# Optimization experiments

Hardware: AMD Instinct MI355X
Metric: run time of the kernel (lower is better)

## Reference

```python
import jax, jax.numpy as jnp
import numpy as np

B, N, DIM = 2, 2048, 1024
H, DH = 16, 64            # num query heads, head dim (single shared kv head)
CTX_N, CTX_DIM = 256, 1024

def setup_inputs() -> dict:
    key = jax.random.key(0)
    ks = jax.random.split(key, 8)
    s = lambda fan: 1.0 / np.sqrt(fan)
    return {
        'x': jax.random.normal(ks[0], (B, N, DIM), jnp.float32),
        'context': jax.random.normal(ks[1], (B, CTX_N, CTX_DIM), jnp.float32),
        'g1': jnp.ones((DIM,), jnp.float32),
        'Wq': jax.random.normal(ks[2], (DIM, H * DH), jnp.float32) * s(DIM),
        'Wkv': jax.random.normal(ks[3], (DIM, 2 * DH), jnp.float32) * s(DIM),
        'null_kv': jax.random.normal(ks[4], (2, DH), jnp.float32) * s(DH),
        'ctx_g': jnp.ones((CTX_DIM,), jnp.float32),
        'ctx_b': jnp.zeros((CTX_DIM,), jnp.float32),
        'Wc': jax.random.normal(ks[5], (CTX_DIM, 2 * DH), jnp.float32) * s(CTX_DIM),
        'bc': jnp.zeros((2 * DH,), jnp.float32),
        'Wout': jax.random.normal(ks[6], (H * DH, DIM), jnp.float32) * s(H * DH),
        'g2': jnp.ones((DIM,), jnp.float32),
    }

def _ln_g(t, g, eps):
    # custom LayerNorm: scale only, no bias, population variance
    m = jnp.mean(t, axis=-1, keepdims=True)
    v = jnp.var(t, axis=-1, keepdims=True)
    return (t - m) / jnp.sqrt(v + eps) * g

def reference(x, context, g1, Wq, Wkv, null_kv, ctx_g, ctx_b, Wc, bc, Wout, g2):
    b, n, _ = x.shape
    scale = DH ** -0.5
    h = _ln_g(x, g1, 1e-5)                              # [b,n,dim]
    q = (h @ Wq).reshape(b, n, H, DH).transpose(0, 2, 1, 3) * scale  # [b,H,n,d]
    k, v = jnp.split(h @ Wkv, 2, axis=-1)               # each [b,n,d] (single kv head)
    # null kv token
    nk = jnp.broadcast_to(null_kv[0], (b, 1, DH))
    nv = jnp.broadcast_to(null_kv[1], (b, 1, DH))
    k = jnp.concatenate((k, nk), axis=-2)
    v = jnp.concatenate((v, nv), axis=-2)
    # context kv tokens (standard flax LayerNorm: scale+bias, eps=1e-6)
    cm = jnp.mean(context, axis=-1, keepdims=True)
    cv_ = jnp.var(context, axis=-1, keepdims=True)
    ch = (context - cm) / jnp.sqrt(cv_ + 1e-6) * ctx_g + ctx_b
    ck, cvv = jnp.split(ch @ Wc + bc, 2, axis=-1)       # [b,ctx_n,d]
    k = jnp.concatenate((k, ck), axis=-2)               # [b,j,d]
    v = jnp.concatenate((v, cvv), axis=-2)
    sim = jnp.einsum('bhid,bjd->bhij', q, k)            # shared kv head broadcast
    attn = jax.nn.softmax(sim, axis=-1)
    out = jnp.einsum('bhij,bjd->bhid', attn, v)
    out = out.transpose(0, 2, 1, 3).reshape(b, n, H * DH)
    out = out @ Wout
    return _ln_g(out, g2, 1e-5)
```

## Files before the change

### kernel.cpp

```cpp
#include <hip/hip_runtime.h>

typedef __attribute__((ext_vector_type(4)))  float  f32x4;
typedef __attribute__((ext_vector_type(16))) float  f32x16;
typedef __attribute__((ext_vector_type(8)))  short  s16x8;

#define DEVI __device__ __forceinline__

constexpr int Bb   = 2;
constexpr int Nn   = 2048;
constexpr int Hh   = 16;
constexpr int DHc  = 64;
constexpr int CTXN = 256;
constexpr int Jv   = Nn + 1 + CTXN;
constexpr int JP   = 2432;
constexpr int QKVN = Hh*DHc + 2*DHc;

DEVI unsigned short f2bf(float f) {
    union { float f; unsigned u; } v; v.f = f;
    unsigned r = v.u + 0x7fffu + ((v.u >> 16) & 1u);
    return (unsigned short)(r >> 16);
}
DEVI float bf2f(unsigned short h) {
    union { unsigned u; float f; } v; v.u = ((unsigned)h) << 16;
    return v.f;
}
DEVI unsigned cvt_pk_bf(float lo, float hi) {
    unsigned r;
    asm("v_cvt_pk_bf16_f32 %0, %1, %2" : "=v"(r) : "v"(lo), "v"(hi));
    return r;
}
DEVI float exp2v(float x) {
    float r;
    asm("v_exp_f32 %0, %1" : "=v"(r) : "v"(x));
    return r;
}
DEVI void gl_lds16(const void* g, void* l) {
    __builtin_amdgcn_global_load_lds(
        (__attribute__((address_space(1))) void*)g,
        (__attribute__((address_space(3))) void*)l,
        16, 0, 0);
}

__global__ __launch_bounds__(256) void k_pre(const float* __restrict__ Wq,
                                             const float* __restrict__ Wkv,
                                             const float* __restrict__ Wc,
                                             const float* __restrict__ Wout,
                                             const float* __restrict__ x,
                                             const float* __restrict__ ctx,
                                             const float* __restrict__ g1,
                                             const float* __restrict__ cg,
                                             const float* __restrict__ cb,
                                             unsigned short* __restrict__ WqkvT,
                                             unsigned short* __restrict__ WcT,
                                             unsigned short* __restrict__ WoutT,
                                             unsigned short* __restrict__ h,
                                             unsigned short* __restrict__ ch,
                                             float qscale) {
    int bxg = blockIdx.x;
    if (bxg < 2304) {
        __shared__ float tile[32][33];
        int bx = bxg % 72, by = bxg / 72;
        const float* in; unsigned short* out; int C; float scale; int cb_;
        if (bx < 32)      { in = Wq;   out = WqkvT;               C = 1024; scale = qscale; cb_ = bx; }
        else if (bx < 36) { in = Wkv;  out = WqkvT + 1024 * 1024; C = 128;  scale = 1.0f;  cb_ = bx - 32; }
        else if (bx < 40) { in = Wc;   out = WcT;                 C = 128;  scale = 1.0f;  cb_ = bx - 36; }
        else              { in = Wout; out = WoutT;               C = 1024; scale = 1.0f;  cb_ = bx - 40; }
        int tx = threadIdx.x & 31, ty = threadIdx.x >> 5;
        int r0 = by * 32, c0 = cb_ * 32;
#pragma unroll
        for (int i = 0; i < 32; i += 8)
            tile[ty + i][tx] = in[(size_t)(r0 + ty + i) * C + c0 + tx];
        __syncthreads();
#pragma unroll
        for (int i = 0; i < 32; i += 8)
            out[(size_t)(c0 + ty + i) * 1024 + r0 + tx] = f2bf(tile[tx][ty + i] * scale);
    } else {
        int row = bxg - 2304, tid = threadIdx.x;
        bool isx = row < 4096;
        const float* rp = isx ? x + (size_t)row * 1024 : ctx + (size_t)(row - 4096) * 1024;
        const float* g  = isx ? g1 : cg;
        float eps = isx ? 1e-5f : 1e-6f;
        unsigned short* o = isx ? h + (size_t)row * 1024 : ch + (size_t)(row - 4096) * 1024;

        f32x4 v = *(const f32x4*)(rp + tid * 4);
        float s = v.x + v.y + v.z + v.w;
        float q = v.x * v.x + v.y * v.y + v.z * v.z + v.w * v.w;
#pragma unroll
        for (int m = 32; m; m >>= 1) { s += __shfl_down(s, m, 64); q += __shfl_down(q, m, 64); }
        __shared__ float ss[4], sq[4];
        int wid = tid >> 6, lane = tid & 63;
        if (lane == 0) { ss[wid] = s; sq[wid] = q; }
        __syncthreads();
        s = ss[0] + ss[1] + ss[2] + ss[3];
        q = sq[0] + sq[1] + sq[2] + sq[3];
        float mean = s * (1.0f / 1024.0f);
        float var  = q * (1.0f / 1024.0f) - mean * mean;
        float rstd = rsqrtf(var + eps);
        f32x4 gg = *(const f32x4*)(g + tid * 4);
        f32x4 r;
#pragma unroll
        for (int e = 0; e < 4; e++) r[e] = (v[e] - mean) * rstd * gg[e];
        if (!isx) {
            f32x4 bb = *(const f32x4*)(cb + tid * 4);
#pragma unroll
            for (int e = 0; e < 4; e++) r[e] += bb[e];
        }
        uint2 ov = make_uint2(cvt_pk_bf(r[0], r[1]), cvt_pk_bf(r[2], r[3]));
        *(uint2*)(o + tid * 4) = ov;
    }
}

__global__ __launch_bounds__(256) void k_ln_out(const unsigned short* __restrict__ in,
                                                const float* __restrict__ g,
                                                float* __restrict__ out) {
    int row = blockIdx.x, tid = threadIdx.x;
    const unsigned short* rp = in + (size_t)row * 1024;
    uint2 raw = *(const uint2*)(rp + tid * 4);
    f32x4 v;
    v.x = bf2f((unsigned short)(raw.x & 0xffff));
    v.y = bf2f((unsigned short)(raw.x >> 16));
    v.z = bf2f((unsigned short)(raw.y & 0xffff));
    v.w = bf2f((unsigned short)(raw.y >> 16));
    float s = v.x + v.y + v.z + v.w;
    float q = v.x * v.x + v.y * v.y + v.z * v.z + v.w * v.w;
#pragma unroll
    for (int m = 32; m; m >>= 1) { s += __shfl_down(s, m, 64); q += __shfl_down(q, m, 64); }
    __shared__ float ss[4], sq[4];
    int wid = tid >> 6, lane = tid & 63;
    if (lane == 0) { ss[wid] = s; sq[wid] = q; }
    __syncthreads();
    s = ss[0] + ss[1] + ss[2] + ss[3];
    q = sq[0] + sq[1] + sq[2] + sq[3];
    float mean = s * (1.0f / 1024.0f);
    float var  = q * (1.0f / 1024.0f) - mean * mean;
    float rstd = rsqrtf(var + 1e-5f);
    f32x4 gg = *(const f32x4*)(g + tid * 4);
    f32x4 r;
#pragma unroll
    for (int e = 0; e < 4; e++) r[e] = (v[e] - mean) * rstd * gg[e];
    *(f32x4*)(out + (size_t)row * 1024 + tid * 4) = r;
}

template<int OUT_BF16>
DEVI void gemm_core(unsigned short* SAb, unsigned short* SBb,
                    const unsigned short* __restrict__ A,
                    const unsigned short* __restrict__ BT,
                    void* __restrict__ C,
                    int M, int N, int K, int bn, int bm) {
    int tid = threadIdx.x;
    int wid = tid >> 6, lane = tid & 63;
    int wm = wid >> 1, wn = wid & 1;
    int lr = lane & 15, lg = lane >> 4;
    int r8 = lane >> 3;
    int sl = (lane & 7) ^ r8;

    const unsigned short* Ag = A  + (size_t)(bm * 128 + wid * 32 + r8) * K + sl * 8;
    const unsigned short* Bg = BT + (size_t)(bn * 64  + wid * 16 + r8) * K + sl * 8;

    auto stage = [&](int buf, int s) {
        int k0 = s << 6;
        unsigned short* SA = SAb + buf * (128 * 64);
        unsigned short* SB = SBb + buf * (64 * 64);
#pragma unroll
        for (int i = 0; i < 4; i++)
            gl_lds16(Ag + (size_t)i * 8 * K + k0, SA + wid * 2048 + i * 512);
#pragma unroll
        for (int i = 0; i < 2; i++)
            gl_lds16(Bg + (size_t)i * 8 * K + k0, SB + wid * 1024 + i * 512);
    };

    f32x4 acc[4][2] = {};
    int nk = K >> 6;
    stage(0, 0);
    stage(1, 1);
    int b0 = 0;
#pragma unroll 1
    for (int s = 0; s < nk; ++s) {
        int b2 = b0 + 2; if (b2 >= 3) b2 -= 3;
        if (s + 2 < nk) {
            stage(b2, s + 2);
            asm volatile("s_waitcnt vmcnt(12)" ::: "memory");
        } else if (s + 1 < nk) {
            asm volatile("s_waitcnt vmcnt(6)" ::: "memory");
        } else {
            asm volatile("s_waitcnt vmcnt(0)" ::: "memory");
        }
        __builtin_amdgcn_s_barrier();
        __builtin_amdgcn_sched_barrier(0);
        const unsigned short* Al = SAb + b0 * (128 * 64);
        const unsigned short* Bl = SBb + b0 * (64 * 64);
#pragma unroll
        for (int kk = 0; kk < 2; kk++) {
            int co = ((kk * 4 + lg) ^ (lr & 7)) * 8;
            s16x8 af[4], bf[2];
#pragma unroll
            for (int mi = 0; mi < 4; mi++)
                af[mi] = *(const s16x8*)&Al[(wm * 64 + mi * 16 + lr) * 64 + co];
#pragma unroll
            for (int ni = 0; ni < 2; ni++)
                bf[ni] = *(const s16x8*)&Bl[(wn * 32 + ni * 16 + lr) * 64 + co];
#pragma unroll
            for (int mi = 0; mi < 4; mi++)
#pragma unroll
                for (int ni = 0; ni < 2; ni++)
                    acc[mi][ni] = __builtin_amdgcn_mfma_f32_16x16x32_bf16(af[mi], bf[ni], acc[mi][ni], 0, 0, 0);
        }
        __builtin_amdgcn_sched_barrier(0);
        __builtin_amdgcn_s_barrier();
        b0 = b0 + 1; if (b0 >= 3) b0 = 0;
    }
#pragma unroll
    for (int mi = 0; mi < 4; mi++)
#pragma unroll
        for (int r = 0; r < 4; r++) {
            int row = bm * 128 + wm * 64 + mi * 16 + lg * 4 + r;
#pragma unroll
            for (int ni = 0; ni < 2; ni++) {
                int col = bn * 64 + wn * 32 + ni * 16 + lr;
                float val = acc[mi][ni][r];
                if (OUT_BF16)
                    ((unsigned short*)C)[(size_t)row * N + col] = f2bf(val);
                else
                    ((float*)C)[(size_t)row * N + col] = val;
            }
        }
}

__global__ __launch_bounds__(256) void k_gemm_qkv(const unsigned short* __restrict__ h,
                                                  const unsigned short* __restrict__ WqkvT,
                                                  unsigned short* __restrict__ qkv,
                                                  const unsigned short* __restrict__ ch,
                                                  const unsigned short* __restrict__ WcT,
                                                  unsigned short* __restrict__ ckv) {
    __shared__ unsigned short SA[3][128 * 64];
    __shared__ unsigned short SB[3][64 * 64];
    int id = blockIdx.x;
    if (id < 576)
        gemm_core<1>(&SA[0][0], &SB[0][0], h, WqkvT, qkv, 4096, 1152, 1024, id % 18, id / 18);
    else {
        int i2 = id - 576;
        gemm_core<1>(&SA[0][0], &SB[0][0], ch, WcT, ckv, 512, 128, 1024, i2 % 2, i2 / 2);
    }
}

__global__ __launch_bounds__(256) void k_gemm_out(const unsigned short* __restrict__ aout,
                                                  const unsigned short* __restrict__ WoutT,
                                                  unsigned short* __restrict__ preout) {
    __shared__ unsigned short SA[3][128 * 64];
    __shared__ unsigned short SB[3][64 * 64];
    int id = blockIdx.x;
    gemm_core<1>(&SA[0][0], &SB[0][0], aout, WoutT, preout, 4096, 1024, 1024, id % 16, id / 16);
}

__global__ __launch_bounds__(256) void k_assemble_kv(const unsigned short* __restrict__ qkv,
                                                     const unsigned short* __restrict__ ckv,
                                                     const float* __restrict__ nkv,
                                                     const float* __restrict__ bc,
                                                     unsigned short* __restrict__ Kb,
                                                     unsigned short* __restrict__ Vt) {
    int idx = blockIdx.x * 256 + threadIdx.x;
    int d = idx & 63;
    int j = (idx >> 6) % JP;
    int b = idx / (64 * JP);
    float kv, vv;
    if (j < Nn) {
        const unsigned short* r = qkv + (size_t)(b * Nn + j) * QKVN + Hh * DHc;
        kv = bf2f(r[d]); vv = bf2f(r[64 + d]);
    } else if (j == Nn) {
        kv = nkv[d]; vv = nkv[64 + d];
    } else if (j < Jv) {
        const unsigned short* r = ckv + (size_t)(b * CTXN + (j - Nn - 1)) * 128;
        kv = bf2f(r[d]) + bc[d]; vv = bf2f(r[64 + d]) + bc[64 + d];
    } else {
        kv = 0.0f; vv = 0.0f;
    }
    Kb[((size_t)b * JP + j) * 64 + d] = f2bf(kv);
    Vt[((size_t)b * 64 + d) * JP + j] = f2bf(vv);
}

__global__ __launch_bounds__(512) void k_attn(const unsigned short* __restrict__ qkv,
                                              const unsigned short* __restrict__ Kb,
                                              const unsigned short* __restrict__ Vt,
                                              unsigned short* __restrict__ aout) {
    __shared__ unsigned short KV[2][2][2][64 * 64];

    int bid = blockIdx.x;
    int qt = bid & 15, h = (bid >> 4) & 15, b = bid >> 8;
    int tid = threadIdx.x, wid = tid >> 6, lane = tid & 63;
    int tm = wid >> 2, tw = wid & 3;
    int l31 = lane & 31, hi = lane >> 5;
    int n0 = qt * 128 + tw * 32;
    int r8 = lane >> 3;
    int sl = (lane & 7) ^ r8;
    int x7 = l31 & 7;
    int jb = tm * 1216;

    s16x8 qf[4];
#pragma unroll
    for (int kk = 0; kk < 4; kk++)
        qf[kk] = *(const s16x8*)(qkv + (size_t)(b * Nn + n0 + l31) * QKVN + h * 64 + kk * 16 + hi * 8);

    f32x16 O0 = {}, O1 = {};
    float Lv = 0.0f;

    const unsigned short* Kg = Kb + ((size_t)b * JP + jb + tw * 16 + r8) * 64 + sl * 8;
    const unsigned short* Vg = Vt + ((size_t)b * 64 + tw * 16 + r8) * JP + jb + sl * 8;

    auto stage = [&](int t, int buf) {
#pragma unroll
        for (int i = 0; i < 2; i++) {
            gl_lds16(Kg + ((size_t)t * 64 + i * 8) * 64, &KV[tm][buf][0][tw * 1024 + i * 512]);
            gl_lds16(Vg + (size_t)i * 8 * JP + t * 64,   &KV[tm][buf][1][tw * 1024 + i * 512]);
        }
    };

    auto build_pf = [&](const f32x16& s, int w) -> s16x8 {
        unsigned c0 = cvt_pk_bf(s[8 * w + 0], s[8 * w + 1]);
        unsigned c1 = cvt_pk_bf(s[8 * w + 2], s[8 * w + 3]);
        unsigned c2 = cvt_pk_bf(s[8 * w + 4], s[8 * w + 5]);
        unsigned c3 = cvt_pk_bf(s[8 * w + 6], s[8 * w + 7]);
        asm("v_permlane32_swap_b32 %0, %1" : "+v"(c0), "+v"(c2));
        asm("v_permlane32_swap_b32 %0, %1" : "+v"(c1), "+v"(c3));
        union { unsigned u[4]; s16x8 v; } pu;
        pu.u[0] = c0; pu.u[1] = c1; pu.u[2] = c2; pu.u[3] = c3;
        return pu.v;
    };

    stage(0, 0);
    asm volatile("s_waitcnt vmcnt(0)" ::: "memory");
    asm volatile("s_barrier" ::: "memory");
    int cur = 0;
#pragma unroll 1
    for (int t = 0; t < 19; ++t) {
        if (t < 18) {
            stage(t + 1, cur ^ 1);
            asm volatile("s_waitcnt vmcnt(4)" ::: "memory");
        } else {
            asm volatile("s_waitcnt vmcnt(0)" ::: "memory");
        }
        asm volatile("s_barrier" ::: "memory");
        __builtin_amdgcn_sched_barrier(0);
        const unsigned short* Kl = &KV[tm][cur][0][0];
        const unsigned short* Vl = &KV[tm][cur][1][0];
        int j0 = jb + t * 64;

        f32x16 s0 = {}, s1 = {};
        __builtin_amdgcn_s_setprio(1);
#pragma unroll
        for (int kk = 0; kk < 4; kk++) {
            int co = ((kk * 2 + hi) ^ x7) * 8;
            s16x8 k0 = *(const s16x8*)&Kl[l31 * 64 + co];
            s16x8 k1 = *(const s16x8*)&Kl[(32 + l31) * 64 + co];
            s0 = __builtin_amdgcn_mfma_f32_32x32x16_bf16(k0, qf[kk], s0, 0, 0, 0);
            s1 = __builtin_amdgcn_mfma_f32_32x32x16_bf16(k1, qf[kk], s1, 0, 0, 0);
        }
        __builtin_amdgcn_s_setprio(0);
        if (j0 + 64 > Jv) {
#pragma unroll
            for (int r = 0; r < 16; r++) {
                int ja = j0 + (r & 3) + 8 * (r >> 2) + 4 * hi;
                if (ja >= Jv)      s0[r] = -1e30f;
                if (ja + 32 >= Jv) s1[r] = -1e30f;
            }
        }

        float sum = 0.0f;
#pragma unroll
        for (int r = 0; r < 16; r++) { s0[r] = exp2v(s0[r]); sum += s0[r]; }
#pragma unroll
        for (int r = 0; r < 16; r++) { s1[r] = exp2v(s1[r]); sum += s1[r]; }
        Lv += sum;

        __builtin_amdgcn_s_setprio(1);
#pragma unroll
        for (int ks = 0; ks < 4; ks++) {
            s16x8 pf = (ks < 2) ? build_pf(s0, ks & 1) : build_pf(s1, ks & 1);
            int co = ((ks * 2 + hi) ^ x7) * 8;
            s16x8 v0 = *(const s16x8*)&Vl[l31 * 64 + co];
            s16x8 v1 = *(const s16x8*)&Vl[(32 + l31) * 64 + co];
            O0 = __builtin_amdgcn_mfma_f32_32x32x16_bf16(v0, pf, O0, 0, 0, 0);
            O1 = __builtin_amdgcn_mfma_f32_32x32x16_bf16(v1, pf, O1, 0, 0, 0);
        }
        __builtin_amdgcn_s_setprio(0);
        __builtin_amdgcn_sched_barrier(0);
        asm volatile("s_barrier" ::: "memory");
        cur ^= 1;
    }

    Lv += __shfl_xor(Lv, 32, 64);

    float* Ob = (float*)&KV[0][0][0][0];
    float* Ml = Ob + 4 * 64 * 33;
    unsigned short* slabs = (unsigned short*)(Ml + 4 * 64);

    __syncthreads();
    if (tm == 1) {
        float* dst = Ob + ((size_t)tw * 64 + lane) * 33;
#pragma unroll
        for (int r = 0; r < 16; r++) { dst[r] = O0[r]; dst[16 + r] = O1[r]; }
        Ml[tw * 64 + lane] = Lv;
    }
    __syncthreads();
    if (tm == 0) {
        const float* src = Ob + ((size_t)tw * 64 + lane) * 33;
        float rl = 1.0f / (Lv + Ml[tw * 64 + lane]);

        unsigned short* slab = slabs + tw * 2304;
#pragma unroll
        for (int rq = 0; rq < 4; rq++) {
            uint2 w0 = make_uint2(
                cvt_pk_bf((O0[rq * 4 + 0] + src[rq * 4 + 0]) * rl,
                          (O0[rq * 4 + 1] + src[rq * 4 + 1]) * rl),
                cvt_pk_bf((O0[rq * 4 + 2] + src[rq * 4 + 2]) * rl,
                          (O0[rq * 4 + 3] + src[rq * 4 + 3]) * rl));
            *(uint2*)&slab[l31 * 72 + rq * 8 + hi * 4] = w0;
            uint2 w1 = make_uint2(
                cvt_pk_bf((O1[rq * 4 + 0] + src[16 + rq * 4 + 0]) * rl,
                          (O1[rq * 4 + 1] + src[16 + rq * 4 + 1]) * rl),
                cvt_pk_bf((O1[rq * 4 + 2] + src[16 + rq * 4 + 2]) * rl,
                          (O1[rq * 4 + 3] + src[16 + rq * 4 + 3]) * rl));
            *(uint2*)&slab[l31 * 72 + 32 + rq * 8 + hi * 4] = w1;
        }
        int q = lane >> 1, half = lane & 1;
        const s16x8* srcq = (const s16x8*)&slab[q * 72 + half * 32];
        s16x8 o0 = srcq[0], o1 = srcq[1], o2 = srcq[2], o3 = srcq[3];
        unsigned short* gdst = aout + (size_t)(b * Nn + n0 + q) * 1024 + h * 64 + half * 32;
        *(s16x8*)gdst = o0;
        *((s16x8*)gdst + 1) = o1;
        *((s16x8*)gdst + 2) = o2;
        *((s16x8*)gdst + 3) = o3;
    }
}

extern "C" void kernel_launch(void* const* d_in, const int* in_sizes, int n_in,
                              void* d_out, int out_size, void* d_ws, size_t ws_size,
                              hipStream_t stream) {
    const float* x    = (const float*)d_in[0];
    const float* ctx  = (const float*)d_in[1];
    const float* g1   = (const float*)d_in[2];
    const float* Wq   = (const float*)d_in[3];
    const float* Wkv  = (const float*)d_in[4];
    const float* nkv  = (const float*)d_in[5];
    const float* ctxg = (const float*)d_in[6];
    const float* ctxb = (const float*)d_in[7];
    const float* Wc   = (const float*)d_in[8];
    const float* bc   = (const float*)d_in[9];
    const float* Wout = (const float*)d_in[10];
    const float* g2   = (const float*)d_in[11];
    float* out = (float*)d_out;

    char* w = (char*)d_ws;
    unsigned short* h_    = (unsigned short*)w; w += (size_t)4096 * 1024 * 2;
    unsigned short* ch    = (unsigned short*)w; w += (size_t)512 * 1024 * 2;
    unsigned short* WqkvT = (unsigned short*)w; w += (size_t)1152 * 1024 * 2;
    unsigned short* WcT   = (unsigned short*)w; w += (size_t)128 * 1024 * 2;
    unsigned short* WoutT = (unsigned short*)w; w += (size_t)1024 * 1024 * 2;
    unsigned short* qkv   = (unsigned short*)w; w += (size_t)4096 * 1152 * 2;
    unsigned short* ckv   = (unsigned short*)w; w += (size_t)512 * 128 * 2;
    unsigned short* Kb    = (unsigned short*)w; w += (size_t)Bb * JP * 64 * 2;
    unsigned short* Vt    = (unsigned short*)w; w += (size_t)Bb * 64 * JP * 2;
    unsigned short* aout  = (unsigned short*)w; w += (size_t)4096 * 1024 * 2;

    const float qscale = 0.125f * 1.4426950408889634f;

    k_pre<<<6912, 256, 0, stream>>>(Wq, Wkv, Wc, Wout, x, ctx, g1, ctxg, ctxb,
                                    WqkvT, WcT, WoutT, h_, ch, qscale);

    k_gemm_qkv<<<584, 256, 0, stream>>>(h_, WqkvT, qkv, ch, WcT, ckv);

    k_assemble_kv<<<(Bb * JP * 64) / 256, 256, 0, stream>>>(qkv, ckv, nkv, bc, Kb, Vt);

    k_attn<<<Bb * Hh * (Nn / 128), 512, 0, stream>>>(qkv, Kb, Vt, aout);

    k_gemm_out<<<512, 256, 0, stream>>>(aout, WoutT, h_);
    k_ln_out<<<4096, 256, 0, stream>>>(h_, g2, out);
}
```

Measured before the change: 115.1 us.

## Switch GEMMs to 128x128 tiles and drop triple-buffered LDS pipeline

Replaces the 128x64 triple-buffered GEMM core with a 128x128 tile kernel that loads A and B into a single LDS buffer, with a sync before and after each load. The larger tile doubles MFMA work per LDS load and halves the block count for the QKV and output projections. In exchange it loses the async prefetch overlap, since each k-step now waits on its own global-to-LDS loads. On a 256-CU device it also leaves fewer blocks (292 and 256) to fill the machine.

```diff
diff --git a/kernel.cpp b/kernel.cpp
--- a/kernel.cpp
+++ b/kernel.cpp
@@ -142,11 +142,11 @@
 }
 
 template<int OUT_BF16>
-DEVI void gemm_core(unsigned short* SAb, unsigned short* SBb,
-                    const unsigned short* __restrict__ A,
-                    const unsigned short* __restrict__ BT,
-                    void* __restrict__ C,
-                    int M, int N, int K, int bn, int bm) {
+DEVI void gemm128(unsigned short* Al, unsigned short* Bl,
+                  const unsigned short* __restrict__ A,
+                  const unsigned short* __restrict__ BT,
+                  void* __restrict__ C,
+                  int M, int N, int K, int bn, int bm) {
     int tid = threadIdx.x;
     int wid = tid >> 6, lane = tid & 63;
     int wm = wid >> 1, wn = wid & 1;
@@ -155,59 +155,36 @@
     int sl = (lane & 7) ^ r8;
 
     const unsigned short* Ag = A  + (size_t)(bm * 128 + wid * 32 + r8) * K + sl * 8;
-    const unsigned short* Bg = BT + (size_t)(bn * 64  + wid * 16 + r8) * K + sl * 8;
-
-    auto stage = [&](int buf, int s) {
-        int k0 = s << 6;
-        unsigned short* SA = SAb + buf * (128 * 64);
-        unsigned short* SB = SBb + buf * (64 * 64);
-#pragma unroll
-        for (int i = 0; i < 4; i++)
-            gl_lds16(Ag + (size_t)i * 8 * K + k0, SA + wid * 2048 + i * 512);
-#pragma unroll
-        for (int i = 0; i < 2; i++)
-            gl_lds16(Bg + (size_t)i * 8 * K + k0, SB + wid * 1024 + i * 512);
-    };
-
-    f32x4 acc[4][2] = {};
+    const unsigned short* Bg = BT + (size_t)(bn * 128 + wid * 32 + r8) * K + sl * 8;
+
+    f32x4 acc[4][4] = {};
     int nk = K >> 6;
-    stage(0, 0);
-    stage(1, 1);
-    int b0 = 0;
 #pragma unroll 1
     for (int s = 0; s < nk; ++s) {
-        int b2 = b0 + 2; if (b2 >= 3) b2 -= 3;
-        if (s + 2 < nk) {
-            stage(b2, s + 2);
-            asm volatile("s_waitcnt vmcnt(12)" ::: "memory");
-        } else if (s + 1 < nk) {
-            asm volatile("s_waitcnt vmcnt(6)" ::: "memory");
-        } else {
-            asm volatile("s_waitcnt vmcnt(0)" ::: "memory");
-        }
-        __builtin_amdgcn_s_barrier();
-        __builtin_amdgcn_sched_barrier(0);
-        const unsigned short* Al = SAb + b0 * (128 * 64);
-        const unsigned short* Bl = SBb + b0 * (64 * 64);
+        int k0 = s << 6;
+        __syncthreads();
+#pragma unroll
+        for (int i = 0; i < 4; i++) {
+            gl_lds16(Ag + (size_t)i * 8 * K + k0, Al + wid * 2048 + i * 512);
+            gl_lds16(Bg + (size_t)i * 8 * K + k0, Bl + wid * 2048 + i * 512);
+        }
+        __syncthreads();
 #pragma unroll
         for (int kk = 0; kk < 2; kk++) {
             int co = ((kk * 4 + lg) ^ (lr & 7)) * 8;
-            s16x8 af[4], bf[2];
+            s16x8 af[4], bf[4];
 #pragma unroll
             for (int mi = 0; mi < 4; mi++)
                 af[mi] = *(const s16x8*)&Al[(wm * 64 + mi * 16 + lr) * 64 + co];
 #pragma unroll
-            for (int ni = 0; ni < 2; ni++)
-                bf[ni] = *(const s16x8*)&Bl[(wn * 32 + ni * 16 + lr) * 64 + co];
+            for (int ni = 0; ni < 4; ni++)
+                bf[ni] = *(const s16x8*)&Bl[(wn * 64 + ni * 16 + lr) * 64 + co];
 #pragma unroll
             for (int mi = 0; mi < 4; mi++)
 #pragma unroll
-                for (int ni = 0; ni < 2; ni++)
+                for (int ni = 0; ni < 4; ni++)
                     acc[mi][ni] = __builtin_amdgcn_mfma_f32_16x16x32_bf16(af[mi], bf[ni], acc[mi][ni], 0, 0, 0);
         }
-        __builtin_amdgcn_sched_barrier(0);
-        __builtin_amdgcn_s_barrier();
-        b0 = b0 + 1; if (b0 >= 3) b0 = 0;
     }
 #pragma unroll
     for (int mi = 0; mi < 4; mi++)
@@ -215,8 +192,8 @@
         for (int r = 0; r < 4; r++) {
             int row = bm * 128 + wm * 64 + mi * 16 + lg * 4 + r;
 #pragma unroll
-            for (int ni = 0; ni < 2; ni++) {
-                int col = bn * 64 + wn * 32 + ni * 16 + lr;
+            for (int ni = 0; ni < 4; ni++) {
+                int col = bn * 128 + wn * 64 + ni * 16 + lr;
                 float val = acc[mi][ni][r];
                 if (OUT_BF16)
                     ((unsigned short*)C)[(size_t)row * N + col] = f2bf(val);
@@ -232,24 +209,22 @@
                                                   const unsigned short* __restrict__ ch,
                                                   const unsigned short* __restrict__ WcT,
                                                   unsigned short* __restrict__ ckv) {
-    __shared__ unsigned short SA[3][128 * 64];
-    __shared__ unsigned short SB[3][64 * 64];
+    __shared__ unsigned short SA[128 * 64];
+    __shared__ unsigned short SB[128 * 64];
     int id = blockIdx.x;
-    if (id < 576)
-        gemm_core<1>(&SA[0][0], &SB[0][0], h, WqkvT, qkv, 4096, 1152, 1024, id % 18, id / 18);
-    else {
-        int i2 = id - 576;
-        gemm_core<1>(&SA[0][0], &SB[0][0], ch, WcT, ckv, 512, 128, 1024, i2 % 2, i2 / 2);
-    }
+    if (id < 288)
+        gemm128<1>(SA, SB, h, WqkvT, qkv, 4096, 1152, 1024, id % 9, id / 9);
+    else
+        gemm128<1>(SA, SB, ch, WcT, ckv, 512, 128, 1024, 0, id - 288);
 }
 
 __global__ __launch_bounds__(256) void k_gemm_out(const unsigned short* __restrict__ aout,
                                                   const unsigned short* __restrict__ WoutT,
                                                   unsigned short* __restrict__ preout) {
-    __shared__ unsigned short SA[3][128 * 64];
-    __shared__ unsigned short SB[3][64 * 64];
+    __shared__ unsigned short SA[128 * 64];
+    __shared__ unsigned short SB[128 * 64];
     int id = blockIdx.x;
-    gemm_core<1>(&SA[0][0], &SB[0][0], aout, WoutT, preout, 4096, 1024, 1024, id % 16, id / 16);
+    gemm128<1>(SA, SB, aout, WoutT, preout, 4096, 1024, 1024, id % 8, id / 8);
 }
 
 __global__ __launch_bounds__(256) void k_assemble_kv(const unsigned short* __restrict__ qkv,
@@ -466,12 +441,12 @@
     k_pre<<<6912, 256, 0, stream>>>(Wq, Wkv, Wc, Wout, x, ctx, g1, ctxg, ctxb,
                                     WqkvT, WcT, WoutT, h_, ch, qscale);
 
-    k_gemm_qkv<<<584, 256, 0, stream>>>(h_, WqkvT, qkv, ch, WcT, ckv);
+    k_gemm_qkv<<<292, 256, 0, stream>>>(h_, WqkvT, qkv, ch, WcT, ckv);
 
     k_assemble_kv<<<(Bb * JP * 64) / 256, 256, 0, stream>>>(qkv, ckv, nkv, bc, Kb, Vt);
 
     k_attn<<<Bb * Hh * (Nn / 128), 512, 0, stream>>>(qkv, Kb, Vt, aout);
 
-    k_gemm_out<<<512, 256, 0, stream>>>(aout, WoutT, h_);
+    k_gemm_out<<<256, 256, 0, stream>>>(aout, WoutT, h_);
     k_ln_out<<<4096, 256, 0, stream>>>(h_, g2, out);
 }
```

Measured after the change: 114.7 us. No clear change (-0.3%).
